# Kernel tuning notes

Hardware: AMD Instinct MI355X
Metric: run time of the kernel (lower is better)

Reference implementation:

```python
import jax, jax.numpy as jnp
import numpy as np

HIDDEN, HEADS, KV_HEADS, HEAD_DIM = 2048, 8, 1, 256
B, L = 2, 4096
ROPE_BASE = 10000.0


def _rope_tables(seq_len, dim, offset=0):
    inv_freq = 1.0 / (ROPE_BASE ** (jnp.arange(0, dim, 2, dtype=jnp.float32) / dim))
    t = jnp.arange(offset, offset + seq_len, dtype=jnp.float32)
    freqs = jnp.einsum('l,d->ld', t, inv_freq)          # [L, dim/2]
    emb = jnp.concatenate([freqs, freqs], axis=-1)      # [L, dim]
    return jnp.cos(emb), jnp.sin(emb)


def _rotate_half(x):
    x1, x2 = jnp.split(x, 2, axis=-1)
    return jnp.concatenate([-x2, x1], axis=-1)


def _apply_rope(x, cos, sin):
    # x: [B, H, L, D]; cos/sin: [L, D] broadcast over B, H
    return x * cos + _rotate_half(x) * sin


def setup_inputs() -> dict:
    key = jax.random.key(0)
    ks = jax.random.split(key, 5)
    s = lambda fan_in: 1.0 / np.sqrt(fan_in)
    return {
        'x':   jax.random.normal(ks[0], (B, L, HIDDEN), jnp.float32),
        'q_w': jax.random.normal(ks[1], (HEADS * HEAD_DIM, HIDDEN), jnp.float32) * s(HIDDEN),
        'k_w': jax.random.normal(ks[2], (KV_HEADS * HEAD_DIM, HIDDEN), jnp.float32) * s(HIDDEN),
        'v_w': jax.random.normal(ks[3], (KV_HEADS * HEAD_DIM, HIDDEN), jnp.float32) * s(HIDDEN),
        'o_w': jax.random.normal(ks[4], (HIDDEN, HEADS * HEAD_DIM), jnp.float32) * s(HEADS * HEAD_DIM),
    }


def reference(x, q_w, k_w, v_w, o_w):
    b, l, _ = x.shape
    g = HEADS // KV_HEADS  # kv groups
    # projections (nn.Linear: x @ W^T)
    q = (x @ q_w.T).reshape(b, l, HEADS, HEAD_DIM).transpose(0, 2, 1, 3)      # [B,H,L,D]
    k = (x @ k_w.T).reshape(b, l, KV_HEADS, HEAD_DIM).transpose(0, 2, 1, 3)   # [B,Hk,L,D]
    v = (x @ v_w.T).reshape(b, l, KV_HEADS, HEAD_DIM).transpose(0, 2, 1, 3)
    cos, sin = _rope_tables(l, HEAD_DIM, offset=0)
    q = _apply_rope(q, cos, sin)
    k = _apply_rope(k, cos, sin)
    # GQA attention without materializing repeated KV heads
    qg = q.reshape(b, KV_HEADS, g, l, HEAD_DIM)
    scale = HEAD_DIM ** -0.5
    scores = jnp.einsum('bkgqd,bkld->bkgql', qg, k) * scale                   # [B,Hk,g,L,L]
    attn = jax.nn.softmax(scores.astype(jnp.float32), axis=-1).astype(q.dtype)
    out = jnp.einsum('bkgql,bkld->bkgqd', attn, v)                            # [B,Hk,g,L,D]
    out = out.reshape(b, HEADS, l, HEAD_DIM).transpose(0, 2, 1, 3).reshape(b, l, HEADS * HEAD_DIM)
    return out @ o_w.T
```

## Files before the change

### kernel.cpp

```cpp
#include <hip/hip_runtime.h>
#include <cstdint>

typedef __bf16 bf16x8 __attribute__((ext_vector_type(8)));
typedef float f32x4 __attribute__((ext_vector_type(4)));
typedef float f32x16 __attribute__((ext_vector_type(16)));
typedef short s16x4 __attribute__((ext_vector_type(4)));
typedef int i32x4 __attribute__((ext_vector_type(4)));

static __device__ __forceinline__ short bf_bits(float f) {
  uint32_t u = __builtin_bit_cast(uint32_t, f);
  u += 0x7fffu + ((u >> 16) & 1u);
  return (short)(u >> 16);
}
static __device__ __forceinline__ float bf_f(short s) {
  uint32_t u = ((uint32_t)(uint16_t)s) << 16;
  return __builtin_bit_cast(float, u);
}
static __device__ __forceinline__ bf16x8 ld_frag(const short* p) {
  i32x4 v = *reinterpret_cast<const i32x4*>(p);
  return __builtin_bit_cast(bf16x8, v);
}

typedef __attribute__((address_space(3))) uint32_t lds_u32_t;
typedef const __attribute__((address_space(1))) uint32_t glb_u32_t;
static __device__ __forceinline__ void gl_lds16(const void* g, const void* l) {
  __builtin_amdgcn_global_load_lds((glb_u32_t*)g,
                                   (lds_u32_t*)(uint32_t)(uintptr_t)l,
                                   16, 0, 0);
}

__global__ void cvt_bf16(const float* __restrict__ in, short* __restrict__ out, int n4) {
  int i = blockIdx.x * blockDim.x + threadIdx.x;
  if (i >= n4) return;
  float4 v = reinterpret_cast<const float4*>(in)[i];
  s16x4 o = { bf_bits(v.x), bf_bits(v.y), bf_bits(v.z), bf_bits(v.w) };
  reinterpret_cast<s16x4*>(out)[i] = o;
}

__global__ void rope_table(float* __restrict__ ct, float* __restrict__ st) {
  int i = blockIdx.x * 256 + threadIdx.x;
  int l = i >> 7, d = i & 127;
  float inv = expf(-0.07195578415625f * (float)d);
  float f = (float)l * inv;
  ct[i] = cosf(f);
  st[i] = sinf(f);
}

__global__ void rope_apply(short* __restrict__ buf, const float* __restrict__ ct,
                           const float* __restrict__ st, int cbase, int hbits,
                           float scale, int total) {
  int i = blockIdx.x * blockDim.x + threadIdx.x;
  if (i >= total) return;
  int dg = i & 31;
  int h = (i >> 5) & ((1 << hbits) - 1);
  int tok = i >> (5 + hbits);
  int l = tok & 4095;
  long base = (long)tok * 2560 + cbase + h * 256;
  int d = dg * 4;
  s16x4 x1 = *reinterpret_cast<const s16x4*>(buf + base + d);
  s16x4 x2 = *reinterpret_cast<const s16x4*>(buf + base + d + 128);
  float4 c = *reinterpret_cast<const float4*>(ct + l * 128 + d);
  float4 s = *reinterpret_cast<const float4*>(st + l * 128 + d);
  s16x4 o1, o2;
  o1.x = bf_bits((bf_f(x1.x) * c.x - bf_f(x2.x) * s.x) * scale);
  o1.y = bf_bits((bf_f(x1.y) * c.y - bf_f(x2.y) * s.y) * scale);
  o1.z = bf_bits((bf_f(x1.z) * c.z - bf_f(x2.z) * s.z) * scale);
  o1.w = bf_bits((bf_f(x1.w) * c.w - bf_f(x2.w) * s.w) * scale);
  o2.x = bf_bits((bf_f(x2.x) * c.x + bf_f(x1.x) * s.x) * scale);
  o2.y = bf_bits((bf_f(x2.y) * c.y + bf_f(x1.y) * s.y) * scale);
  o2.z = bf_bits((bf_f(x2.z) * c.z + bf_f(x1.z) * s.z) * scale);
  o2.w = bf_bits((bf_f(x2.w) * c.w + bf_f(x1.w) * s.w) * scale);
  *reinterpret_cast<s16x4*>(buf + base + d) = o1;
  *reinterpret_cast<s16x4*>(buf + base + d + 128) = o2;
}

__global__ void transpose_v(const short* __restrict__ qkv, short* __restrict__ vt) {
  int i = blockIdx.x * 256 + threadIdx.x;
  int d = i & 255;
  int lg = (i >> 8) & 511;
  int b = i >> 17;
  const short* src = qkv + ((long)b * 4096 + lg * 8) * 2560 + 2304 + d;
  short tmp[8];
  #pragma unroll
  for (int j = 0; j < 8; ++j) tmp[j] = src[(long)j * 2560];
  short* dst = vt + ((long)b * 256 + d) * 4096 + lg * 8;
  s16x4 lo = { tmp[0], tmp[1], tmp[2], tmp[3] };
  s16x4 hi4 = { tmp[4], tmp[5], tmp[6], tmp[7] };
  *reinterpret_cast<s16x4*>(dst) = lo;
  *reinterpret_cast<s16x4*>(dst + 4) = hi4;
}

template <bool OUT_F32>
__global__ __launch_bounds__(256) void gemm_bt(const short* __restrict__ A,
                                               const short* __restrict__ B,
                                               void* __restrict__ C,
                                               int K, int ldc) {
  __shared__ short As[128 * 32];
  __shared__ short Bs[128 * 32];
  const int t = threadIdx.x;
  const int lane = t & 63;
  const int w = t >> 6;
  const long m0 = (long)blockIdx.x * 128;
  const long n0 = (long)blockIdx.y * 128;
  const int wr = (w >> 1) * 64, wc = (w & 1) * 64;
  const int fr = lane & 15, fk = (lane >> 4) * 8;
  f32x4 acc[4][4] = {};

  for (int k0 = 0; k0 < K; k0 += 32) {
    #pragma unroll
    for (int p = 0; p < 2; ++p) {
      int idx = p * 256 + t;
      gl_lds16(A + (m0 + (idx >> 2)) * K + k0 + (idx & 3) * 8, As + idx * 8);
    }
    #pragma unroll
    for (int p = 0; p < 2; ++p) {
      int idx = p * 256 + t;
      gl_lds16(B + (n0 + (idx >> 2)) * K + k0 + (idx & 3) * 8, Bs + idx * 8);
    }
    __syncthreads();
    bf16x8 af[4], bfr[4];
    #pragma unroll
    for (int i = 0; i < 4; ++i) af[i] = ld_frag(As + (wr + i * 16 + fr) * 32 + fk);
    #pragma unroll
    for (int j = 0; j < 4; ++j) bfr[j] = ld_frag(Bs + (wc + j * 16 + fr) * 32 + fk);
    #pragma unroll
    for (int i = 0; i < 4; ++i)
      #pragma unroll
      for (int j = 0; j < 4; ++j)
        acc[i][j] = __builtin_amdgcn_mfma_f32_16x16x32_bf16(af[i], bfr[j], acc[i][j], 0, 0, 0);
    __syncthreads();
  }
  const int er = lane >> 4, ec = lane & 15;
  #pragma unroll
  for (int i = 0; i < 4; ++i)
    #pragma unroll
    for (int j = 0; j < 4; ++j) {
      long col = n0 + wc + j * 16 + ec;
      #pragma unroll
      for (int r = 0; r < 4; ++r) {
        long row = m0 + wr + i * 16 + er * 4 + r;
        if constexpr (OUT_F32)
          reinterpret_cast<float*>(C)[row * ldc + col] = acc[i][j][r];
        else
          reinterpret_cast<short*>(C)[row * ldc + col] = bf_bits(acc[i][j][r]);
      }
    }
}

__global__ __launch_bounds__(256, 2) void attn(const short* __restrict__ qkv,
                                               const short* __restrict__ vtg,
                                               short* __restrict__ og) {
  __shared__ __align__(16) short KtS[2 * 32 * 256];
  __shared__ __align__(16) short VtS[2 * 256 * 32];
  const int t = threadIdx.x;
  const int lane = t & 63, w = t >> 6;
  const int lq = lane & 31, hi = lane >> 5;
  const int u = blockIdx.x;
  const int b = (u >> 2) & 1;
  const int local = (u & 3) | ((u >> 3) << 2);
  const int h = local >> 5;
  const int q0 = (local & 31) * 128;

  bf16x8 Qf[16];
  {
    const short* qp = qkv + ((long)(b * 4096 + q0 + w * 32 + lq)) * 2560 + h * 256;
    #pragma unroll
    for (int ds = 0; ds < 16; ++ds) Qf[ds] = ld_frag(qp + ds * 16 + hi * 8);
  }

  const short* kptr[4];
  const short* vptr[4];
  #pragma unroll
  for (int p = 0; p < 4; ++p) {
    int c = p * 256 + t;
    int r = c >> 5, s = c & 31;
    kptr[p] = qkv + ((long)(b * 4096 + r)) * 2560 + 2048 + ((s ^ (r & 7)) * 8);
  }
  #pragma unroll
  for (int p = 0; p < 4; ++p) {
    int c = p * 256 + t;
    int d = c >> 2, s = c & 3;
    vptr[p] = vtg + ((long)(b * 256 + d)) * 4096 + ((s ^ ((d >> 1) & 3)) * 8);
  }

#define STAGE(BUF) do {                                                          \
    _Pragma("unroll")                                                            \
    for (int p = 0; p < 4; ++p)                                                  \
      gl_lds16(kptr[p], KtS + (BUF) * 8192 + (p * 256 + t) * 8);                 \
    _Pragma("unroll")                                                            \
    for (int p = 0; p < 4; ++p)                                                  \
      gl_lds16(vptr[p], VtS + (BUF) * 8192 + (p * 256 + t) * 8);                 \
    _Pragma("unroll")                                                            \
    for (int p = 0; p < 4; ++p) { kptr[p] += 32 * 2560; vptr[p] += 32; }         \
  } while (0)

  STAGE(0);
  __syncthreads();

  f32x16 Oa[8] = {};
  float mrun = -3.0e38f, lrun = 0.0f;
  const int xk8 = (lq & 7) * 8;
  const int xv8 = ((lq >> 1) & 3) * 8;
  const int lv32 = lq * 32;
  int cur = 0;

  for (int kv0 = 0; kv0 < 4096; kv0 += 32) {
    if (kv0 + 32 < 4096) STAGE(cur ^ 1);
    const short* Kc = KtS + cur * 8192;
    const short* Vc = VtS + cur * 8192;

    f32x16 S = {};
    #pragma unroll
    for (int ds = 0; ds < 16; ++ds) {
      bf16x8 a = ld_frag(Kc + lq * 256 + ((ds * 16 + hi * 8) ^ xk8));
      S = __builtin_amdgcn_mfma_f32_32x32x16_bf16(a, Qf[ds], S, 0, 0, 0);
    }
    float smax = S[0];
    #pragma unroll
    for (int r = 1; r < 16; ++r) smax = fmaxf(smax, S[r]);
    smax = fmaxf(smax, __shfl_xor(smax, 32));

    if (__any(smax > mrun + 8.0f)) {
      float mnew = fmaxf(mrun, smax);
      float alpha = __expf(mrun - mnew);
      #pragma unroll
      for (int r = 0; r < 16; ++r) {
        int qp2 = (r & 3) + 8 * (r >> 2) + 4 * hi;
        float ar = __shfl(alpha, qp2);
        #pragma unroll
        for (int df = 0; df < 8; ++df) Oa[df][r] *= ar;
      }
      lrun *= alpha;
      mrun = mnew;
    }
    float psum = 0.0f;
    #pragma unroll
    for (int r = 0; r < 16; ++r) { S[r] = __expf(S[r] - mrun); psum += S[r]; }
    psum += __shfl_xor(psum, 32);
    lrun += psum;

    bf16x8 pa[2];
    #pragma unroll
    for (int kvs = 0; kvs < 2; ++kvs) {
      uint32_t x0, x1, y0, y1;
      asm("v_cvt_pk_bf16_f32 %0, %1, %2" : "=v"(x0) : "v"(S[8 * kvs + 0]), "v"(S[8 * kvs + 1]));
      asm("v_cvt_pk_bf16_f32 %0, %1, %2" : "=v"(x1) : "v"(S[8 * kvs + 2]), "v"(S[8 * kvs + 3]));
      asm("v_cvt_pk_bf16_f32 %0, %1, %2" : "=v"(y0) : "v"(S[8 * kvs + 4]), "v"(S[8 * kvs + 5]));
      asm("v_cvt_pk_bf16_f32 %0, %1, %2" : "=v"(y1) : "v"(S[8 * kvs + 6]), "v"(S[8 * kvs + 7]));
      asm("v_permlane32_swap_b32 %0, %1" : "+v"(x0), "+v"(y0));
      asm("v_permlane32_swap_b32 %0, %1" : "+v"(x1), "+v"(y1));
      i32x4 wv = { (int)x0, (int)x1, (int)y0, (int)y1 };
      pa[kvs] = __builtin_bit_cast(bf16x8, wv);
    }

    #pragma unroll
    for (int df = 0; df < 8; ++df)
      #pragma unroll
      for (int kvs = 0; kvs < 2; ++kvs) {
        bf16x8 vb = ld_frag(Vc + df * 1024 + lv32 + ((kvs * 16 + hi * 8) ^ xv8));
        Oa[df] = __builtin_amdgcn_mfma_f32_32x32x16_bf16(pa[kvs], vb, Oa[df], 0, 0, 0);
      }

    __syncthreads();
    cur ^= 1;
  }
#undef STAGE

  float linv = 1.0f / lrun;
  float lir[16];
  #pragma unroll
  for (int r = 0; r < 16; ++r) {
    int qp2 = (r & 3) + 8 * (r >> 2) + 4 * hi;
    lir[r] = __shfl(linv, qp2);
  }
  short* ob = og + ((long)(b * 4096 + q0)) * 2048 + h * 256;
  short* chunk = KtS;
  #pragma unroll
  for (int half = 0; half < 2; ++half) {
    __syncthreads();
    #pragma unroll
    for (int df4 = 0; df4 < 4; ++df4) {
      #pragma unroll
      for (int r = 0; r < 16; ++r) {
        int qp2 = (r & 3) + 8 * (r >> 2) + 4 * hi;
        chunk[(w * 32 + qp2) * 128 + df4 * 32 + lq] = bf_bits(Oa[half * 4 + df4][r] * lir[r]);
      }
    }
    __syncthreads();
    #pragma unroll
    for (int p = 0; p < 8; ++p) {
      int idx = p * 256 + t, row = idx >> 4, dg = idx & 15;
      i32x4 val = *reinterpret_cast<const i32x4*>(chunk + row * 128 + dg * 8);
      *reinterpret_cast<i32x4*>(ob + (long)row * 2048 + half * 128 + dg * 8) = val;
    }
  }
}

extern "C" void kernel_launch(void* const* d_in, const int* in_sizes, int n_in,
                              void* d_out, int out_size, void* d_ws, size_t ws_size,
                              hipStream_t stream) {
  const float* x  = (const float*)d_in[0];
  const float* qw = (const float*)d_in[1];
  const float* kw = (const float*)d_in[2];
  const float* vw = (const float*)d_in[3];
  const float* ow = (const float*)d_in[4];
  float* out = (float*)d_out;
  char* ws = (char*)d_ws;

  short* xb  = (short*)(ws);
  short* wb  = (short*)(ws + 33554432);
  short* qkv = (short*)(ws + 44040192);
  short* vtb = (short*)(ws + 85983232);
  float* ct  = (float*)(ws + 90177536);
  float* st  = (float*)(ws + 92274688);
  short* wob = (short*)(ws + 94371840);

  cvt_bf16<<<16384, 256, 0, stream>>>(x,  xb, 4194304);
  cvt_bf16<<<4096,  256, 0, stream>>>(qw, wb, 1048576);
  cvt_bf16<<<512,   256, 0, stream>>>(kw, wb + 2048 * 2048, 131072);
  cvt_bf16<<<512,   256, 0, stream>>>(vw, wb + 2304 * 2048, 131072);
  cvt_bf16<<<4096,  256, 0, stream>>>(ow, wob, 1048576);
  rope_table<<<2048, 256, 0, stream>>>(ct, st);

  gemm_bt<false><<<dim3(64, 20), 256, 0, stream>>>(xb, wb, qkv, 2048, 2560);

  rope_apply<<<8192, 256, 0, stream>>>(qkv, ct, st, 0,    3, 0.0625f, 2097152);
  rope_apply<<<1024, 256, 0, stream>>>(qkv, ct, st, 2048, 0, 1.0f,    262144);
  transpose_v<<<1024, 256, 0, stream>>>(qkv, vtb);

  attn<<<512, 256, 0, stream>>>(qkv, vtb, xb);

  gemm_bt<true><<<dim3(64, 16), 256, 0, stream>>>(xb, wob, out, 2048, 2048);
}
```

Before: 639.1 us.

## Prefetch two KV tiles ahead with explicit vmcnt waits and MFMA priority

Restructures the KV staging so that two tiles are in flight: both buffers are prefilled, and after each tile is consumed it is refilled with the tile two steps ahead, with partial s_waitcnt vmcnt(8) instead of full syncs. This lets global-to-LDS loads overlap more of the compute. The QK^T MFMA chain is also split into two independent accumulators to break the dependency chain, reductions become tree-shaped, and s_setprio raises wave priority around the MFMA blocks. The change relies on exact vmcnt counts and adds an extra barrier per iteration.

```diff
diff --git a/kernel.cpp b/kernel.cpp
--- a/kernel.cpp
+++ b/kernel.cpp
@@ -183,19 +183,19 @@
     vptr[p] = vtg + ((long)(b * 256 + d)) * 4096 + ((s ^ ((d >> 1) & 3)) * 8);
   }
 
-#define STAGE(BUF) do {                                                          \
+#define STAGE(BUF, T0) do {                                                      \
     _Pragma("unroll")                                                            \
     for (int p = 0; p < 4; ++p)                                                  \
-      gl_lds16(kptr[p], KtS + (BUF) * 8192 + (p * 256 + t) * 8);                 \
+      gl_lds16(kptr[p] + (long)(T0) * 2560, KtS + (BUF) * 8192 + (p * 256 + t) * 8); \
     _Pragma("unroll")                                                            \
     for (int p = 0; p < 4; ++p)                                                  \
-      gl_lds16(vptr[p], VtS + (BUF) * 8192 + (p * 256 + t) * 8);                 \
-    _Pragma("unroll")                                                            \
-    for (int p = 0; p < 4; ++p) { kptr[p] += 32 * 2560; vptr[p] += 32; }         \
+      gl_lds16(vptr[p] + (T0), VtS + (BUF) * 8192 + (p * 256 + t) * 8);          \
   } while (0)
 
-  STAGE(0);
-  __syncthreads();
+  STAGE(0, 0);
+  STAGE(1, 32);
+  asm volatile("s_waitcnt vmcnt(8)" ::: "memory");
+  __builtin_amdgcn_s_barrier();
 
   f32x16 Oa[8] = {};
   float mrun = -3.0e38f, lrun = 0.0f;
@@ -205,19 +205,28 @@
   int cur = 0;
 
   for (int kv0 = 0; kv0 < 4096; kv0 += 32) {
-    if (kv0 + 32 < 4096) STAGE(cur ^ 1);
     const short* Kc = KtS + cur * 8192;
     const short* Vc = VtS + cur * 8192;
 
-    f32x16 S = {};
-    #pragma unroll
-    for (int ds = 0; ds < 16; ++ds) {
-      bf16x8 a = ld_frag(Kc + lq * 256 + ((ds * 16 + hi * 8) ^ xk8));
-      S = __builtin_amdgcn_mfma_f32_32x32x16_bf16(a, Qf[ds], S, 0, 0, 0);
-    }
-    float smax = S[0];
-    #pragma unroll
-    for (int r = 1; r < 16; ++r) smax = fmaxf(smax, S[r]);
+    f32x16 S0 = {}, S1 = {};
+    __builtin_amdgcn_s_setprio(1);
+    #pragma unroll
+    for (int ds = 0; ds < 8; ++ds) {
+      bf16x8 a0 = ld_frag(Kc + lq * 256 + ((ds * 16 + hi * 8) ^ xk8));
+      bf16x8 a1 = ld_frag(Kc + lq * 256 + (((ds + 8) * 16 + hi * 8) ^ xk8));
+      S0 = __builtin_amdgcn_mfma_f32_32x32x16_bf16(a0, Qf[ds], S0, 0, 0, 0);
+      S1 = __builtin_amdgcn_mfma_f32_32x32x16_bf16(a1, Qf[ds + 8], S1, 0, 0, 0);
+    }
+    __builtin_amdgcn_s_setprio(0);
+    f32x16 S;
+    #pragma unroll
+    for (int r = 0; r < 16; ++r) S[r] = S0[r] + S1[r];
+
+    float t8[8];
+    #pragma unroll
+    for (int r = 0; r < 8; ++r) t8[r] = fmaxf(S[r], S[r + 8]);
+    float smax = fmaxf(fmaxf(fmaxf(t8[0], t8[4]), fmaxf(t8[1], t8[5])),
+                       fmaxf(fmaxf(t8[2], t8[6]), fmaxf(t8[3], t8[7])));
     smax = fmaxf(smax, __shfl_xor(smax, 32));
 
     if (__any(smax > mrun + 8.0f)) {
@@ -233,9 +242,12 @@
       lrun *= alpha;
       mrun = mnew;
     }
-    float psum = 0.0f;
-    #pragma unroll
-    for (int r = 0; r < 16; ++r) { S[r] = __expf(S[r] - mrun); psum += S[r]; }
+    #pragma unroll
+    for (int r = 0; r < 16; ++r) S[r] = __expf(S[r] - mrun);
+    float p8[8];
+    #pragma unroll
+    for (int r = 0; r < 8; ++r) p8[r] = S[r] + S[r + 8];
+    float psum = (p8[0] + p8[4]) + (p8[1] + p8[5]) + ((p8[2] + p8[6]) + (p8[3] + p8[7]));
     psum += __shfl_xor(psum, 32);
     lrun += psum;
 
@@ -253,6 +265,7 @@
       pa[kvs] = __builtin_bit_cast(bf16x8, wv);
     }
 
+    __builtin_amdgcn_s_setprio(1);
     #pragma unroll
     for (int df = 0; df < 8; ++df)
       #pragma unroll
@@ -260,8 +273,16 @@
         bf16x8 vb = ld_frag(Vc + df * 1024 + lv32 + ((kvs * 16 + hi * 8) ^ xv8));
         Oa[df] = __builtin_amdgcn_mfma_f32_32x32x16_bf16(pa[kvs], vb, Oa[df], 0, 0, 0);
       }
-
-    __syncthreads();
+    __builtin_amdgcn_s_setprio(0);
+
+    __builtin_amdgcn_s_barrier();
+    if (kv0 + 64 < 4096) {
+      STAGE(cur, kv0 + 64);
+      asm volatile("s_waitcnt vmcnt(8)" ::: "memory");
+    } else {
+      asm volatile("s_waitcnt vmcnt(0)" ::: "memory");
+    }
+    __builtin_amdgcn_s_barrier();
     cur ^= 1;
   }
 #undef STAGE
```

Measured after the change: 769.3 us. 1.2x slower.
